# Kernel optimization log

Hardware: AMD Instinct MI355X
Metric: run time of the kernel (lower is better)

## Reference

```python
import jax, jax.numpy as jnp
import numpy as np

B, F, D = 16384, 256, 128
H = [512, 256]
OUT = 8
VOCAB = 100000


def setup_inputs() -> dict:
    key = jax.random.key(0)
    ks = jax.random.split(key, 16)
    s = lambda k, *sh: jax.random.normal(k, sh, jnp.float32) * 0.05
    return dict(
        features=jax.random.normal(ks[0], (B, F), jnp.float32),
        ent_idx=jax.random.randint(ks[1], (B,), 0, VOCAB),
        target=jax.random.randint(ks[2], (B,), 0, OUT),
        Wf=s(ks[3], F, D), bf=jnp.zeros((D,), jnp.float32),
        Wu=s(ks[4], D, D), bu=jnp.zeros((D,), jnp.float32),
        w_cf=s(ks[5], D), w_fc=s(ks[6], D),
        w_ef=s(ks[7], D), w_fe=s(ks[8], D),
        b_c=jnp.zeros((1,), jnp.float32), b_e=jnp.zeros((1,), jnp.float32),
        head_tab=s(ks[9], VOCAB, D), ent_tab=s(ks[10], VOCAB, D),
        W0=s(ks[11], 2 * D, H[0]), b0=jnp.zeros((H[0],), jnp.float32),
        W1=s(ks[12], H[0], H[1]), b1=jnp.zeros((H[1],), jnp.float32),
        W2=s(ks[13], H[1], OUT), b2=jnp.zeros((OUT,), jnp.float32),
    )


def cross_compress(f, e, w_cf, w_fc, w_ef, w_fe, b_c, b_e):
    # torch code builds c = f (outer) e of shape (B,D,D) then matmuls a (D,1)
    # vector; algebraically (f e^T) w = f * (e . w), so we use the O(B*D) form.
    ew_cf = e @ w_cf  # (B,)
    fw_fc = f @ w_fc
    ew_ef = e @ w_ef
    fw_fe = f @ w_fe
    new_f = f * ew_cf[:, None] + e * fw_fc[:, None] + b_c
    new_e = f * ew_ef[:, None] + e * fw_fe[:, None] + b_e
    return new_f, new_e


def reference(features, ent_idx, target, Wf, bf, Wu, bu, w_cf, w_fc, w_ef,
              w_fe, b_c, b_e, head_tab, ent_tab, W0, b0, W1, b1, W2, b2):
    # 'rec' branch of CompanyOperationEvaluation.forward (eval mode, dropout=id)
    cf = jax.nn.relu(features @ Wf + bf)          # feature_layer
    e = ent_tab[ent_idx]                           # entity_embed lookup
    h = head_tab[ent_idx]                          # head_embed lookup (same ids)
    for _ in range(2):
        cf = jax.nn.relu(cf @ Wu + bu)             # user_low_mlp_layer
        h, e = cross_compress(h, e, w_cf, w_fc, w_ef, w_fe, b_c, b_e)
    high = jnp.concatenate([cf, e], axis=1)        # (B, 2D)
    x = jax.nn.relu(high @ W0 + b0)
    x = jax.nn.relu(x @ W1 + b1)
    x = jax.nn.relu(x @ W2 + b2)                   # pred_last_layer
    prob = jax.nn.softmax(x, axis=1)
    return (prob, target)
```

## Files before the change

### kernel.cpp

```cpp
#include <hip/hip_runtime.h>
#include <hip/hip_bf16.h>


typedef __bf16 bf16x8 __attribute__((ext_vector_type(8)));
typedef float floatx4 __attribute__((ext_vector_type(4)));

__device__ __forceinline__ unsigned short f2bf(float x) {
  unsigned int u = __builtin_bit_cast(unsigned int, x);
  u = (u + 0x7FFFu + ((u >> 16) & 1u)) >> 16;
  return (unsigned short)u;
}

__global__ __launch_bounds__(256) void prep_kernel(
    const int* __restrict__ ent_idx, const float* __restrict__ head_tab,
    const float* __restrict__ ent_tab,
    const float* __restrict__ w_cf, const float* __restrict__ w_fc,
    const float* __restrict__ w_ef, const float* __restrict__ w_fe,
    const float* __restrict__ b_c, const float* __restrict__ b_e,
    const float* __restrict__ Wf, const float* __restrict__ Wu,
    const float* __restrict__ W0, const float* __restrict__ W1,
    const float* __restrict__ W2,
    unsigned short* __restrict__ high,
    unsigned short* __restrict__ wfT, unsigned short* __restrict__ wuT,
    unsigned short* __restrict__ w0T, unsigned short* __restrict__ w1T,
    unsigned short* __restrict__ w2T) {
  __shared__ unsigned short tile[32][34];
  const int bid = blockIdx.x, tid = threadIdx.x;
  if (bid < 2048) {
    const int row = bid * 8 + (tid >> 5);
    const int c = (tid & 31) * 4;
    const int idx = ent_idx[row];
    float4 hv = *(const float4*)(head_tab + (size_t)idx * 128 + c);
    float4 ev = *(const float4*)(ent_tab + (size_t)idx * 128 + c);
    float h[4] = {hv.x, hv.y, hv.z, hv.w};
    float e[4] = {ev.x, ev.y, ev.z, ev.w};
    float wcf[4], wfc[4], wef[4], wfe[4];
#pragma unroll
    for (int j = 0; j < 4; ++j) {
      wcf[j] = w_cf[c + j]; wfc[j] = w_fc[c + j];
      wef[j] = w_ef[c + j]; wfe[j] = w_fe[c + j];
    }
    const float bc = b_c[0], be = b_e[0];
#pragma unroll
    for (int it = 0; it < 2; ++it) {
      float d0 = 0, d1 = 0, d2 = 0, d3 = 0;
#pragma unroll
      for (int j = 0; j < 4; ++j) {
        d0 += e[j] * wcf[j]; d1 += h[j] * wfc[j];
        d2 += e[j] * wef[j]; d3 += h[j] * wfe[j];
      }
#pragma unroll
      for (int s = 1; s < 32; s <<= 1) {
        d0 += __shfl_xor(d0, s); d1 += __shfl_xor(d1, s);
        d2 += __shfl_xor(d2, s); d3 += __shfl_xor(d3, s);
      }
      float nh[4], ne[4];
#pragma unroll
      for (int j = 0; j < 4; ++j) {
        nh[j] = h[j] * d0 + e[j] * d1 + bc;
        ne[j] = h[j] * d2 + e[j] * d3 + be;
      }
#pragma unroll
      for (int j = 0; j < 4; ++j) { h[j] = nh[j]; e[j] = ne[j]; }
    }
    uint2 v;
    v.x = (unsigned)f2bf(e[0]) | ((unsigned)f2bf(e[1]) << 16);
    v.y = (unsigned)f2bf(e[2]) | ((unsigned)f2bf(e[3]) << 16);
    *(uint2*)(high + (size_t)row * 256 + 128 + c) = v;
  } else if (bid < 2352) {
    int t = bid - 2048;
    const float* src; unsigned short* dst; int N, K, kt, nt;
    if (t < 32)       { src = Wf; dst = wfT; N = 128; K = 256; kt = t >> 2;       nt = t & 3; }
    else if (t < 48)  { t -= 32;  src = Wu; dst = wuT; N = 128; K = 128; kt = t >> 2; nt = t & 3; }
    else if (t < 176) { t -= 48;  src = W0; dst = w0T; N = 512; K = 256; kt = t >> 4; nt = t & 15; }
    else              { t -= 176; src = W1; dst = w1T; N = 256; K = 512; kt = t >> 3; nt = t & 7; }
    {
      int r = tid >> 3, cg = (tid & 7) * 4;
      float4 v = *(const float4*)(src + (size_t)(kt * 32 + r) * N + nt * 32 + cg);
      tile[r][cg + 0] = f2bf(v.x); tile[r][cg + 1] = f2bf(v.y);
      tile[r][cg + 2] = f2bf(v.z); tile[r][cg + 3] = f2bf(v.w);
    }
    __syncthreads();
    {
      int rp = tid >> 3, cg = (tid & 7) * 4;
      uint2 o;
      o.x = (unsigned)tile[cg + 0][rp] | ((unsigned)tile[cg + 1][rp] << 16);
      o.y = (unsigned)tile[cg + 2][rp] | ((unsigned)tile[cg + 3][rp] << 16);
      *(uint2*)(dst + (size_t)(nt * 32 + rp) * K + kt * 32 + cg) = o;
    }
  } else {
#pragma unroll
    for (int i = 0; i < 8; ++i) {
      int g = tid * 8 + i, k = g >> 3, n = g & 7;
      w2T[n * 256 + k] = f2bf(W2[g]);
    }
  }
}

template <int LDA>
__device__ __forceinline__ void layer32(const unsigned short* A_sh,
                                        const unsigned short* __restrict__ BT,
                                        int K, unsigned short* b_sh,
                                        floatx4 acc[2][2]) {
  const int tid = threadIdx.x, lane = tid & 63, wave = tid >> 6;
  const int m16 = lane & 15, quad = lane >> 4;
#pragma unroll
  for (int mi = 0; mi < 2; ++mi)
#pragma unroll
    for (int ni = 0; ni < 2; ++ni) acc[mi][ni] = (floatx4){0.f, 0.f, 0.f, 0.f};
  for (int k0 = 0; k0 < K; k0 += 64) {
    __syncthreads();
#pragma unroll
    for (int i = 0; i < 4; ++i) {
      int chunk = i * 256 + tid;
      int row = chunk >> 3, seg = chunk & 7;
      *(uint4*)&b_sh[row * 72 + seg * 8] =
          *(const uint4*)(BT + (size_t)row * K + k0 + seg * 8);
    }
    __syncthreads();
#pragma unroll
    for (int kk = 0; kk < 64; kk += 32) {
      bf16x8 a[2], b[2];
#pragma unroll
      for (int mi = 0; mi < 2; ++mi)
        a[mi] = *(const bf16x8*)&A_sh[(mi * 16 + m16) * LDA + k0 + kk + quad * 8];
#pragma unroll
      for (int ni = 0; ni < 2; ++ni)
        b[ni] = *(const bf16x8*)&b_sh[(wave * 32 + ni * 16 + m16) * 72 + kk + quad * 8];
#pragma unroll
      for (int mi = 0; mi < 2; ++mi)
#pragma unroll
        for (int ni = 0; ni < 2; ++ni)
          acc[mi][ni] = __builtin_amdgcn_mfma_f32_16x16x32_bf16(a[mi], b[ni], acc[mi][ni], 0, 0, 0);
    }
  }
  __syncthreads();
}

__global__ __launch_bounds__(256) void fused_mlp_kernel(
    const float* __restrict__ features, const unsigned short* __restrict__ wfT,
    const unsigned short* __restrict__ wuT, const float* __restrict__ bf_,
    const float* __restrict__ bu, const unsigned short* __restrict__ high,
    const unsigned short* __restrict__ w0T, const float* __restrict__ b0,
    const unsigned short* __restrict__ w1T, const float* __restrict__ b1,
    const unsigned short* __restrict__ w2T, const float* __restrict__ b2,
    const int* __restrict__ target, float* __restrict__ out) {
  __shared__ __align__(16) unsigned short regionA[17152];
  __shared__ __align__(16) unsigned short b_sh[256 * 72];
  __shared__ __align__(16) unsigned short w2_sh[2048];
  unsigned short* feat_sh = regionA;
  unsigned short* buf0 = regionA + 8448;
  unsigned short* buf1 = regionA + 12800;
  unsigned short* A_sh = regionA;
  unsigned short* x0_sh = regionA;
  unsigned short* x1_sh = b_sh;

  const int tid = threadIdx.x;
  const int r0 = blockIdx.x * 32;
  *(uint4*)&w2_sh[tid * 8] = *(const uint4*)(w2T + tid * 8);

#pragma unroll
  for (int i = 0; i < 8; ++i) {
    int idx4 = i * 256 + tid;
    int row = idx4 >> 6, c = (idx4 & 63) * 4;
    float4 v = *(const float4*)(features + (size_t)(r0 + row) * 256 + c);
    uint2 o;
    o.x = (unsigned)f2bf(v.x) | ((unsigned)f2bf(v.y) << 16);
    o.y = (unsigned)f2bf(v.z) | ((unsigned)f2bf(v.w) << 16);
    *(uint2*)&feat_sh[row * 264 + c] = o;
  }
  const int lane = tid & 63, wave = tid >> 6;
  const int m16 = lane & 15, quad = lane >> 4;
  floatx4 acc[2][2];

  layer32<264>(feat_sh, wfT, 256, b_sh, acc);
#pragma unroll
  for (int mi = 0; mi < 2; ++mi)
#pragma unroll
    for (int ni = 0; ni < 2; ++ni) {
      int col = wave * 32 + ni * 16 + m16;
      float bv = bf_[col];
#pragma unroll
      for (int r = 0; r < 4; ++r)
        buf0[(mi * 16 + quad * 4 + r) * 136 + col] =
            f2bf(fmaxf(acc[mi][ni][r] + bv, 0.f));
    }
#pragma unroll
  for (int i = 0; i < 2; ++i) {
    int idx = i * 256 + tid;
    int row = idx >> 4, seg = idx & 15;
    *(uint4*)&A_sh[row * 264 + 128 + seg * 8] =
        *(const uint4*)(high + (size_t)(r0 + row) * 256 + 128 + seg * 8);
  }
  layer32<136>(buf0, wuT, 128, b_sh, acc);
#pragma unroll
  for (int mi = 0; mi < 2; ++mi)
#pragma unroll
    for (int ni = 0; ni < 2; ++ni) {
      int col = wave * 32 + ni * 16 + m16;
      float bv = bu[col];
#pragma unroll
      for (int r = 0; r < 4; ++r)
        buf1[(mi * 16 + quad * 4 + r) * 136 + col] =
            f2bf(fmaxf(acc[mi][ni][r] + bv, 0.f));
    }
  layer32<136>(buf1, wuT, 128, b_sh, acc);
#pragma unroll
  for (int mi = 0; mi < 2; ++mi)
#pragma unroll
    for (int ni = 0; ni < 2; ++ni) {
      int col = wave * 32 + ni * 16 + m16;
      float bv = bu[col];
#pragma unroll
      for (int r = 0; r < 4; ++r)
        A_sh[(mi * 16 + quad * 4 + r) * 264 + col] =
            f2bf(fmaxf(acc[mi][ni][r] + bv, 0.f));
    }

  floatx4 acc8[2][8];
#pragma unroll
  for (int mi = 0; mi < 2; ++mi)
#pragma unroll
    for (int ni = 0; ni < 8; ++ni) acc8[mi][ni] = (floatx4){0.f, 0.f, 0.f, 0.f};
  for (int k0 = 0; k0 < 256; k0 += 64) {
#pragma unroll
    for (int nh = 0; nh < 2; ++nh) {
      __syncthreads();
#pragma unroll
      for (int i = 0; i < 8; ++i) {
        int chunk = i * 256 + tid;
        int row = chunk >> 3, seg = chunk & 7;
        *(uint4*)&b_sh[row * 72 + seg * 8] =
            *(const uint4*)(w0T + (size_t)(nh * 256 + row) * 256 + k0 + seg * 8);
      }
      __syncthreads();
#pragma unroll
      for (int kk = 0; kk < 64; kk += 32) {
        bf16x8 a[2], b[4];
#pragma unroll
        for (int mi = 0; mi < 2; ++mi)
          a[mi] = *(const bf16x8*)&A_sh[(mi * 16 + m16) * 264 + k0 + kk + quad * 8];
#pragma unroll
        for (int ni = 0; ni < 4; ++ni)
          b[ni] = *(const bf16x8*)&b_sh[(wave * 64 + ni * 16 + m16) * 72 + kk + quad * 8];
#pragma unroll
        for (int mi = 0; mi < 2; ++mi)
#pragma unroll
          for (int ni = 0; ni < 4; ++ni)
            acc8[mi][nh * 4 + ni] = __builtin_amdgcn_mfma_f32_16x16x32_bf16(
                a[mi], b[ni], acc8[mi][nh * 4 + ni], 0, 0, 0);
      }
    }
  }
  __syncthreads();
#pragma unroll
  for (int mi = 0; mi < 2; ++mi)
#pragma unroll
    for (int nh = 0; nh < 2; ++nh)
#pragma unroll
      for (int ni = 0; ni < 4; ++ni) {
        int col = nh * 256 + wave * 64 + ni * 16 + m16;
        float bv = b0[col];
#pragma unroll
        for (int r = 0; r < 4; ++r)
          x0_sh[(mi * 16 + quad * 4 + r) * 520 + col] =
              f2bf(fmaxf(acc8[mi][nh * 4 + ni][r] + bv, 0.f));
      }

  floatx4 acc4[2][4];
#pragma unroll
  for (int mi = 0; mi < 2; ++mi)
#pragma unroll
    for (int ni = 0; ni < 4; ++ni) acc4[mi][ni] = (floatx4){0.f, 0.f, 0.f, 0.f};
  for (int k0 = 0; k0 < 512; k0 += 64) {
    __syncthreads();
#pragma unroll
    for (int i = 0; i < 8; ++i) {
      int chunk = i * 256 + tid;
      int row = chunk >> 3, seg = chunk & 7;
      *(uint4*)&b_sh[row * 72 + seg * 8] =
          *(const uint4*)(w1T + (size_t)row * 512 + k0 + seg * 8);
    }
    __syncthreads();
#pragma unroll
    for (int kk = 0; kk < 64; kk += 32) {
      bf16x8 a[2], b[4];
#pragma unroll
      for (int mi = 0; mi < 2; ++mi)
        a[mi] = *(const bf16x8*)&x0_sh[(mi * 16 + m16) * 520 + k0 + kk + quad * 8];
#pragma unroll
      for (int ni = 0; ni < 4; ++ni)
        b[ni] = *(const bf16x8*)&b_sh[(wave * 64 + ni * 16 + m16) * 72 + kk + quad * 8];
#pragma unroll
      for (int mi = 0; mi < 2; ++mi)
#pragma unroll
        for (int ni = 0; ni < 4; ++ni)
          acc4[mi][ni] = __builtin_amdgcn_mfma_f32_16x16x32_bf16(a[mi], b[ni], acc4[mi][ni], 0, 0, 0);
    }
  }
  __syncthreads();
#pragma unroll
  for (int mi = 0; mi < 2; ++mi)
#pragma unroll
    for (int ni = 0; ni < 4; ++ni) {
      int col = wave * 64 + ni * 16 + m16;
      float bv = b1[col];
#pragma unroll
      for (int r = 0; r < 4; ++r)
        x1_sh[(mi * 16 + quad * 4 + r) * 264 + col] = f2bf(fmaxf(acc4[mi][ni][r] + bv, 0.f));
    }
  __syncthreads();
  {
    int row = tid >> 3, q = tid & 7;
    float p[8];
#pragma unroll
    for (int n = 0; n < 8; ++n) p[n] = 0.f;
#pragma unroll
    for (int jb = 0; jb < 4; ++jb) {
      bf16x8 xv = *(const bf16x8*)&x1_sh[row * 264 + q * 32 + jb * 8];
#pragma unroll
      for (int n = 0; n < 8; ++n) {
        bf16x8 wv = *(const bf16x8*)&w2_sh[n * 256 + q * 32 + jb * 8];
#pragma unroll
        for (int j = 0; j < 8; ++j) p[n] += (float)xv[j] * (float)wv[j];
      }
    }
#pragma unroll
    for (int s = 1; s < 8; s <<= 1)
#pragma unroll
      for (int n = 0; n < 8; ++n) p[n] += __shfl_xor(p[n], s);
    if (q == 0) {
      float mx = -1e30f;
#pragma unroll
      for (int n = 0; n < 8; ++n) {
        p[n] = fmaxf(p[n] + b2[n], 0.f);
        mx = fmaxf(mx, p[n]);
      }
      float sum = 0.f;
#pragma unroll
      for (int n = 0; n < 8; ++n) { p[n] = __expf(p[n] - mx); sum += p[n]; }
      const float inv = 1.f / sum;
      const int gr = r0 + row;
      float4 o0 = {p[0] * inv, p[1] * inv, p[2] * inv, p[3] * inv};
      float4 o1 = {p[4] * inv, p[5] * inv, p[6] * inv, p[7] * inv};
      *(float4*)(out + (size_t)gr * 8) = o0;
      *(float4*)(out + (size_t)gr * 8 + 4) = o1;
      out[16384 * 8 + gr] = (float)target[gr];
    }
  }
}

extern "C" void kernel_launch(void* const* d_in, const int* in_sizes, int n_in,
                              void* d_out, int out_size, void* d_ws, size_t ws_size,
                              hipStream_t stream) {
  const float* features = (const float*)d_in[0];
  const int* ent_idx    = (const int*)d_in[1];
  const int* target     = (const int*)d_in[2];
  const float* Wf  = (const float*)d_in[3];
  const float* bf_ = (const float*)d_in[4];
  const float* Wu  = (const float*)d_in[5];
  const float* bu  = (const float*)d_in[6];
  const float* w_cf = (const float*)d_in[7];
  const float* w_fc = (const float*)d_in[8];
  const float* w_ef = (const float*)d_in[9];
  const float* w_fe = (const float*)d_in[10];
  const float* b_c  = (const float*)d_in[11];
  const float* b_e  = (const float*)d_in[12];
  const float* head_tab = (const float*)d_in[13];
  const float* ent_tab  = (const float*)d_in[14];
  const float* W0 = (const float*)d_in[15];
  const float* b0 = (const float*)d_in[16];
  const float* W1 = (const float*)d_in[17];
  const float* b1 = (const float*)d_in[18];
  const float* W2 = (const float*)d_in[19];
  const float* b2 = (const float*)d_in[20];
  float* out = (float*)d_out;

  unsigned short* ws = (unsigned short*)d_ws;
  size_t off = 0;
  auto alloc = [&](size_t n) { unsigned short* p = ws + off; off += n; return p; };
  unsigned short* high = alloc(16384ull * 256);
  unsigned short* wfT  = alloc(32768);
  unsigned short* wuT  = alloc(16384);
  unsigned short* w0T  = alloc(131072);
  unsigned short* w1T  = alloc(131072);
  unsigned short* w2T  = alloc(2048);
  (void)ws_size; (void)in_sizes; (void)n_in; (void)out_size;

  prep_kernel<<<2353, 256, 0, stream>>>(ent_idx, head_tab, ent_tab,
      w_cf, w_fc, w_ef, w_fe, b_c, b_e, Wf, Wu, W0, W1, W2,
      high, wfT, wuT, w0T, w1T, w2T);
  fused_mlp_kernel<<<512, 256, 0, stream>>>(features, wfT, wuT, bf_, bu,
      high, w0T, b0, w1T, b1, w2T, b2, target, out);
}
```

Measured before the change: 202.6 us.

## Double-buffer weight tiles with register prefetch across all fused MLP GEMM phases

```diff
diff --git a/kernel.cpp b/kernel.cpp
--- a/kernel.cpp
+++ b/kernel.cpp
@@ -10,6 +10,13 @@
   u = (u + 0x7FFFu + ((u >> 16) & 1u)) >> 16;
   return (unsigned short)u;
 }
+
+#define PHASE_BAR()                                      \
+  do {                                                   \
+    asm volatile("s_waitcnt lgkmcnt(0)" ::: "memory");   \
+    __builtin_amdgcn_s_barrier();                        \
+    __builtin_amdgcn_sched_barrier(0);                   \
+  } while (0)
 
 __global__ __launch_bounds__(256) void prep_kernel(
     const int* __restrict__ ent_idx, const float* __restrict__ head_tab,
@@ -97,47 +104,72 @@
   }
 }
 
+template <int LDK>
+__device__ __forceinline__ void loadB(uint4 (&r)[4],
+                                      const unsigned short* __restrict__ p,
+                                      int tid) {
+#pragma unroll
+  for (int i = 0; i < 4; ++i) {
+    int chunk = i * 256 + tid, row = chunk >> 3, seg = chunk & 7;
+    r[i] = *(const uint4*)(p + (size_t)row * LDK + seg * 8);
+  }
+}
+
+__device__ __forceinline__ void dsw(unsigned short* b, const uint4 (&r)[4],
+                                    int tid) {
+#pragma unroll
+  for (int i = 0; i < 4; ++i) {
+    int chunk = i * 256 + tid, row = chunk >> 3, seg = chunk & 7;
+    *(uint4*)&b[row * 72 + seg * 8] = r[i];
+  }
+}
+
+template <int PASS_STEPS, int LDK>
+__device__ __forceinline__ const unsigned short* srcstep(
+    const unsigned short* __restrict__ s, int st) {
+  return s + (size_t)(st / PASS_STEPS) * 128 * LDK + (st % PASS_STEPS) * 64;
+}
+
 template <int LDA>
-__device__ __forceinline__ void layer32(const unsigned short* A_sh,
-                                        const unsigned short* __restrict__ BT,
-                                        int K, unsigned short* b_sh,
-                                        floatx4 acc[2][2]) {
-  const int tid = threadIdx.x, lane = tid & 63, wave = tid >> 6;
-  const int m16 = lane & 15, quad = lane >> 4;
-#pragma unroll
-  for (int mi = 0; mi < 2; ++mi)
-#pragma unroll
-    for (int ni = 0; ni < 2; ++ni) acc[mi][ni] = (floatx4){0.f, 0.f, 0.f, 0.f};
-  for (int k0 = 0; k0 < K; k0 += 64) {
-    __syncthreads();
-#pragma unroll
-    for (int i = 0; i < 4; ++i) {
-      int chunk = i * 256 + tid;
-      int row = chunk >> 3, seg = chunk & 7;
-      *(uint4*)&b_sh[row * 72 + seg * 8] =
-          *(const uint4*)(BT + (size_t)row * K + k0 + seg * 8);
-    }
-    __syncthreads();
-#pragma unroll
-    for (int kk = 0; kk < 64; kk += 32) {
-      bf16x8 a[2], b[2];
-#pragma unroll
-      for (int mi = 0; mi < 2; ++mi)
-        a[mi] = *(const bf16x8*)&A_sh[(mi * 16 + m16) * LDA + k0 + kk + quad * 8];
-#pragma unroll
-      for (int ni = 0; ni < 2; ++ni)
-        b[ni] = *(const bf16x8*)&b_sh[(wave * 32 + ni * 16 + m16) * 72 + kk + quad * 8];
-#pragma unroll
-      for (int mi = 0; mi < 2; ++mi)
-#pragma unroll
-        for (int ni = 0; ni < 2; ++ni)
-          acc[mi][ni] = __builtin_amdgcn_mfma_f32_16x16x32_bf16(a[mi], b[ni], acc[mi][ni], 0, 0, 0);
-    }
-  }
-  __syncthreads();
-}
-
-__global__ __launch_bounds__(256) void fused_mlp_kernel(
+__device__ __forceinline__ void mstep(const unsigned short* A,
+                                      const unsigned short* b, int k0,
+                                      floatx4* acc, int m16, int quad,
+                                      int wave) {
+#pragma unroll
+  for (int kk = 0; kk < 64; kk += 32) {
+    bf16x8 a0 = *(const bf16x8*)&A[m16 * LDA + k0 + kk + quad * 8];
+    bf16x8 a1 = *(const bf16x8*)&A[(16 + m16) * LDA + k0 + kk + quad * 8];
+    bf16x8 b0 = *(const bf16x8*)&b[(wave * 32 + m16) * 72 + kk + quad * 8];
+    bf16x8 b1 = *(const bf16x8*)&b[(wave * 32 + 16 + m16) * 72 + kk + quad * 8];
+    acc[0] = __builtin_amdgcn_mfma_f32_16x16x32_bf16(a0, b0, acc[0], 0, 0, 0);
+    acc[1] = __builtin_amdgcn_mfma_f32_16x16x32_bf16(a0, b1, acc[1], 0, 0, 0);
+    acc[2] = __builtin_amdgcn_mfma_f32_16x16x32_bf16(a1, b0, acc[2], 0, 0, 0);
+    acc[3] = __builtin_amdgcn_mfma_f32_16x16x32_bf16(a1, b1, acc[3], 0, 0, 0);
+  }
+}
+
+template <int T, int LDA, int PASS_STEPS, int LDK>
+__device__ __forceinline__ void gemm_phase(
+    const unsigned short* A, const unsigned short* __restrict__ src,
+    unsigned short* b_sh, floatx4* acc, int tid, int m16, int quad, int wave) {
+  uint4 r[2][4];
+  loadB<LDK>(r[0], srcstep<PASS_STEPS, LDK>(src, 0), tid);
+  dsw(b_sh, r[0], tid);
+  loadB<LDK>(r[1], srcstep<PASS_STEPS, LDK>(src, 1), tid);
+  PHASE_BAR();
+#pragma unroll
+  for (int t = 0; t < T; ++t) {
+    unsigned short* bcur = b_sh + (t & 1) * 9216;
+    unsigned short* bnxt = b_sh + ((t + 1) & 1) * 9216;
+    if (t + 2 < T) loadB<LDK>(r[t & 1], srcstep<PASS_STEPS, LDK>(src, t + 2), tid);
+    mstep<LDA>(A, bcur, (t % PASS_STEPS) * 64, acc + (t / PASS_STEPS) * 4, m16,
+               quad, wave);
+    if (t + 1 < T) dsw(bnxt, r[(t + 1) & 1], tid);
+    PHASE_BAR();
+  }
+}
+
+__global__ __launch_bounds__(256, 2) void fused_mlp_kernel(
     const float* __restrict__ features, const unsigned short* __restrict__ wfT,
     const unsigned short* __restrict__ wuT, const float* __restrict__ bf_,
     const float* __restrict__ bu, const unsigned short* __restrict__ high,
@@ -146,7 +178,7 @@
     const unsigned short* __restrict__ w2T, const float* __restrict__ b2,
     const int* __restrict__ target, float* __restrict__ out) {
   __shared__ __align__(16) unsigned short regionA[17152];
-  __shared__ __align__(16) unsigned short b_sh[256 * 72];
+  __shared__ __align__(16) unsigned short b_sh[2 * 9216];
   __shared__ __align__(16) unsigned short w2_sh[2048];
   unsigned short* feat_sh = regionA;
   unsigned short* buf0 = regionA + 8448;
@@ -157,6 +189,12 @@
 
   const int tid = threadIdx.x;
   const int r0 = blockIdx.x * 32;
+  const int lane = tid & 63, wave = tid >> 6;
+  const int m16 = lane & 15, quad = lane >> 4;
+
+  const int hrow = tid >> 4, hseg = (tid & 15) * 8;
+  uint4 hv0 = *(const uint4*)(high + (size_t)(r0 + hrow) * 256 + 128 + hseg);
+  uint4 hv1 = *(const uint4*)(high + (size_t)(r0 + 16 + hrow) * 256 + 128 + hseg);
   *(uint4*)&w2_sh[tid * 8] = *(const uint4*)(w2T + tid * 8);
 
 #pragma unroll
@@ -169,11 +207,11 @@
     o.y = (unsigned)f2bf(v.z) | ((unsigned)f2bf(v.w) << 16);
     *(uint2*)&feat_sh[row * 264 + c] = o;
   }
-  const int lane = tid & 63, wave = tid >> 6;
-  const int m16 = lane & 15, quad = lane >> 4;
-  floatx4 acc[2][2];
-
-  layer32<264>(feat_sh, wfT, 256, b_sh, acc);
+
+  floatx4 acc[4];
+#pragma unroll
+  for (int j = 0; j < 4; ++j) acc[j] = (floatx4){0.f, 0.f, 0.f, 0.f};
+  gemm_phase<4, 264, 4, 256>(feat_sh, wfT, b_sh, acc, tid, m16, quad, wave);
 #pragma unroll
   for (int mi = 0; mi < 2; ++mi)
 #pragma unroll
@@ -183,16 +221,14 @@
 #pragma unroll
       for (int r = 0; r < 4; ++r)
         buf0[(mi * 16 + quad * 4 + r) * 136 + col] =
-            f2bf(fmaxf(acc[mi][ni][r] + bv, 0.f));
-    }
-#pragma unroll
-  for (int i = 0; i < 2; ++i) {
-    int idx = i * 256 + tid;
-    int row = idx >> 4, seg = idx & 15;
-    *(uint4*)&A_sh[row * 264 + 128 + seg * 8] =
-        *(const uint4*)(high + (size_t)(r0 + row) * 256 + 128 + seg * 8);
-  }
-  layer32<136>(buf0, wuT, 128, b_sh, acc);
+            f2bf(fmaxf(acc[mi * 2 + ni][r] + bv, 0.f));
+    }
+  *(uint4*)&A_sh[hrow * 264 + 128 + hseg] = hv0;
+  *(uint4*)&A_sh[(16 + hrow) * 264 + 128 + hseg] = hv1;
+
+#pragma unroll
+  for (int j = 0; j < 4; ++j) acc[j] = (floatx4){0.f, 0.f, 0.f, 0.f};
+  gemm_phase<2, 136, 2, 128>(buf0, wuT, b_sh, acc, tid, m16, quad, wave);
 #pragma unroll
   for (int mi = 0; mi < 2; ++mi)
 #pragma unroll
@@ -202,9 +238,12 @@
 #pragma unroll
       for (int r = 0; r < 4; ++r)
         buf1[(mi * 16 + quad * 4 + r) * 136 + col] =
-            f2bf(fmaxf(acc[mi][ni][r] + bv, 0.f));
-    }
-  layer32<136>(buf1, wuT, 128, b_sh, acc);
+            f2bf(fmaxf(acc[mi * 2 + ni][r] + bv, 0.f));
+    }
+
+#pragma unroll
+  for (int j = 0; j < 4; ++j) acc[j] = (floatx4){0.f, 0.f, 0.f, 0.f};
+  gemm_phase<2, 136, 2, 128>(buf1, wuT, b_sh, acc, tid, m16, quad, wave);
 #pragma unroll
   for (int mi = 0; mi < 2; ++mi)
 #pragma unroll
@@ -214,102 +253,46 @@
 #pragma unroll
       for (int r = 0; r < 4; ++r)
         A_sh[(mi * 16 + quad * 4 + r) * 264 + col] =
-            f2bf(fmaxf(acc[mi][ni][r] + bv, 0.f));
-    }
-
-  floatx4 acc8[2][8];
-#pragma unroll
-  for (int mi = 0; mi < 2; ++mi)
-#pragma unroll
-    for (int ni = 0; ni < 8; ++ni) acc8[mi][ni] = (floatx4){0.f, 0.f, 0.f, 0.f};
-  for (int k0 = 0; k0 < 256; k0 += 64) {
-#pragma unroll
-    for (int nh = 0; nh < 2; ++nh) {
-      __syncthreads();
-#pragma unroll
-      for (int i = 0; i < 8; ++i) {
-        int chunk = i * 256 + tid;
-        int row = chunk >> 3, seg = chunk & 7;
-        *(uint4*)&b_sh[row * 72 + seg * 8] =
-            *(const uint4*)(w0T + (size_t)(nh * 256 + row) * 256 + k0 + seg * 8);
-      }
-      __syncthreads();
-#pragma unroll
-      for (int kk = 0; kk < 64; kk += 32) {
-        bf16x8 a[2], b[4];
-#pragma unroll
-        for (int mi = 0; mi < 2; ++mi)
-          a[mi] = *(const bf16x8*)&A_sh[(mi * 16 + m16) * 264 + k0 + kk + quad * 8];
-#pragma unroll
-        for (int ni = 0; ni < 4; ++ni)
-          b[ni] = *(const bf16x8*)&b_sh[(wave * 64 + ni * 16 + m16) * 72 + kk + quad * 8];
-#pragma unroll
-        for (int mi = 0; mi < 2; ++mi)
-#pragma unroll
-          for (int ni = 0; ni < 4; ++ni)
-            acc8[mi][nh * 4 + ni] = __builtin_amdgcn_mfma_f32_16x16x32_bf16(
-                a[mi], b[ni], acc8[mi][nh * 4 + ni], 0, 0, 0);
-      }
-    }
-  }
-  __syncthreads();
-#pragma unroll
-  for (int mi = 0; mi < 2; ++mi)
-#pragma unroll
-    for (int nh = 0; nh < 2; ++nh)
-#pragma unroll
-      for (int ni = 0; ni < 4; ++ni) {
-        int col = nh * 256 + wave * 64 + ni * 16 + m16;
+            f2bf(fmaxf(acc[mi * 2 + ni][r] + bv, 0.f));
+    }
+
+  floatx4 acc16[16];
+#pragma unroll
+  for (int j = 0; j < 16; ++j) acc16[j] = (floatx4){0.f, 0.f, 0.f, 0.f};
+  gemm_phase<16, 264, 4, 256>(A_sh, w0T, b_sh, acc16, tid, m16, quad, wave);
+#pragma unroll
+  for (int np = 0; np < 4; ++np)
+#pragma unroll
+    for (int mi = 0; mi < 2; ++mi)
+#pragma unroll
+      for (int ni = 0; ni < 2; ++ni) {
+        int col = np * 128 + wave * 32 + ni * 16 + m16;
         float bv = b0[col];
 #pragma unroll
         for (int r = 0; r < 4; ++r)
           x0_sh[(mi * 16 + quad * 4 + r) * 520 + col] =
-              f2bf(fmaxf(acc8[mi][nh * 4 + ni][r] + bv, 0.f));
-      }
-
-  floatx4 acc4[2][4];
-#pragma unroll
-  for (int mi = 0; mi < 2; ++mi)
-#pragma unroll
-    for (int ni = 0; ni < 4; ++ni) acc4[mi][ni] = (floatx4){0.f, 0.f, 0.f, 0.f};
-  for (int k0 = 0; k0 < 512; k0 += 64) {
-    __syncthreads();
-#pragma unroll
-    for (int i = 0; i < 8; ++i) {
-      int chunk = i * 256 + tid;
-      int row = chunk >> 3, seg = chunk & 7;
-      *(uint4*)&b_sh[row * 72 + seg * 8] =
-          *(const uint4*)(w1T + (size_t)row * 512 + k0 + seg * 8);
-    }
-    __syncthreads();
-#pragma unroll
-    for (int kk = 0; kk < 64; kk += 32) {
-      bf16x8 a[2], b[4];
-#pragma unroll
-      for (int mi = 0; mi < 2; ++mi)
-        a[mi] = *(const bf16x8*)&x0_sh[(mi * 16 + m16) * 520 + k0 + kk + quad * 8];
-#pragma unroll
-      for (int ni = 0; ni < 4; ++ni)
-        b[ni] = *(const bf16x8*)&b_sh[(wave * 64 + ni * 16 + m16) * 72 + kk + quad * 8];
-#pragma unroll
-      for (int mi = 0; mi < 2; ++mi)
-#pragma unroll
-        for (int ni = 0; ni < 4; ++ni)
-          acc4[mi][ni] = __builtin_amdgcn_mfma_f32_16x16x32_bf16(a[mi], b[ni], acc4[mi][ni], 0, 0, 0);
-    }
-  }
-  __syncthreads();
-#pragma unroll
-  for (int mi = 0; mi < 2; ++mi)
-#pragma unroll
-    for (int ni = 0; ni < 4; ++ni) {
-      int col = wave * 64 + ni * 16 + m16;
-      float bv = b1[col];
-#pragma unroll
-      for (int r = 0; r < 4; ++r)
-        x1_sh[(mi * 16 + quad * 4 + r) * 264 + col] = f2bf(fmaxf(acc4[mi][ni][r] + bv, 0.f));
-    }
-  __syncthreads();
+              f2bf(fmaxf(acc16[np * 4 + mi * 2 + ni][r] + bv, 0.f));
+      }
+
+  floatx4 acc8[8];
+#pragma unroll
+  for (int j = 0; j < 8; ++j) acc8[j] = (floatx4){0.f, 0.f, 0.f, 0.f};
+  gemm_phase<16, 520, 8, 512>(x0_sh, w1T, b_sh, acc8, tid, m16, quad, wave);
+#pragma unroll
+  for (int np = 0; np < 2; ++np)
+#pragma unroll
+    for (int mi = 0; mi < 2; ++mi)
+#pragma unroll
+      for (int ni = 0; ni < 2; ++ni) {
+        int col = np * 128 + wave * 32 + ni * 16 + m16;
+        float bv = b1[col];
+#pragma unroll
+        for (int r = 0; r < 4; ++r)
+          x1_sh[(mi * 16 + quad * 4 + r) * 264 + col] =
+              f2bf(fmaxf(acc8[np * 4 + mi * 2 + ni][r] + bv, 0.f));
+      }
+  PHASE_BAR();
+
   {
     int row = tid >> 3, q = tid & 7;
     float p[8];
```

New measurement: 188.2 us. -7.1%, faster.
